# Kernel optimization log

Hardware: AMD Instinct MI355X
Metric: run time of the kernel (lower is better)

The kernel has to match this reference:

```python
import jax, jax.numpy as jnp
from jax import lax
import numpy as np

B, T, I, H, O = 128, 256, 256, 1024, 128


def _rnn_layer(x, W_ih, W_hh, b_ih, b_hh):
    # x: [B, T, D_in] -> hidden states [B, T, H]
    # precompute input projection for all timesteps (batched GEMM)
    xW = jnp.einsum('btd,hd->bth', x, W_ih) + b_ih + b_hh  # [B, T, H]

    def step(h, xw_t):
        h = jnp.tanh(xw_t + h @ W_hh.T)  # [B, H]
        return h, h

    h0 = jnp.zeros((x.shape[0], W_hh.shape[0]), x.dtype)
    _, hs = lax.scan(step, h0, jnp.swapaxes(xW, 0, 1))  # hs: [T, B, H]
    return jnp.swapaxes(hs, 0, 1)  # [B, T, H]


def setup_inputs() -> dict:
    key = jax.random.key(0)
    ks = jax.random.split(key, 11)
    s_ih0 = 1.0 / np.sqrt(H)
    inp = {
        'X': jax.random.normal(ks[0], (B, T, I), jnp.float32),
        'W_ih0': jax.random.uniform(ks[1], (H, I), jnp.float32, -s_ih0, s_ih0),
        'W_hh0': jax.random.uniform(ks[2], (H, H), jnp.float32, -s_ih0, s_ih0),
        'b_ih0': jax.random.uniform(ks[3], (H,), jnp.float32, -s_ih0, s_ih0),
        'b_hh0': jax.random.uniform(ks[4], (H,), jnp.float32, -s_ih0, s_ih0),
        'W_ih1': jax.random.uniform(ks[5], (H, H), jnp.float32, -s_ih0, s_ih0),
        'W_hh1': jax.random.uniform(ks[6], (H, H), jnp.float32, -s_ih0, s_ih0),
        'b_ih1': jax.random.uniform(ks[7], (H,), jnp.float32, -s_ih0, s_ih0),
        'b_hh1': jax.random.uniform(ks[8], (H,), jnp.float32, -s_ih0, s_ih0),
        'W_fc': jax.random.uniform(ks[9], (O, H), jnp.float32, -s_ih0, s_ih0),
        'b_fc': jax.random.uniform(ks[10], (O,), jnp.float32, -s_ih0, s_ih0),
    }
    return inp


def reference(X, W_ih0, W_hh0, b_ih0, b_hh0, W_ih1, W_hh1, b_ih1, b_hh1, W_fc, b_fc):
    h1 = _rnn_layer(X, W_ih0, W_hh0, b_ih0, b_hh0)   # layer 0: [B, T, H]
    h2 = _rnn_layer(h1, W_ih1, W_hh1, b_ih1, b_hh1)  # layer 1: [B, T, H]
    last = h2[:, -1, :]                               # [B, H]
    return last @ W_fc.T + b_fc                       # [B, O]
```

## Files before the change

kernel.cpp:

```cpp
#include <hip/hip_runtime.h>
#include <stdint.h>
#include <stddef.h>

#define B_ 128
#define T_ 256
#define I_ 256
#define H_ 1024
#define O_ 128

typedef __attribute__((ext_vector_type(8))) __bf16 bf16x8;
typedef __attribute__((ext_vector_type(4))) float f32x4;
typedef unsigned long long u64;
typedef unsigned int u32;



__global__ void split_kernel(const float* __restrict__ src, __bf16* __restrict__ hi,
                             __bf16* __restrict__ lo, int n) {
    int i = blockIdx.x * blockDim.x + threadIdx.x;
    int stride = gridDim.x * blockDim.x;
    for (; i < n; i += stride) {
        float v = src[i];
        __bf16 h = (__bf16)v;
        hi[i] = h;
        lo[i] = (__bf16)(v - (float)h);
    }
}

__global__ void pack_x(const float* __restrict__ X, u32* __restrict__ xp) {
    int i = blockIdx.x * 256 + threadIdx.x;
    int dw   = i & 3;
    int ln   = (i >> 2) & 15;
    int k8   = (i >> 6) & 31;
    int bt16 = (i >> 11) & 7;
    int t    = i >> 14;
    int k = k8 * 8 + dw * 2;
    int b = bt16 * 16 + ln;
    long xo = (long)b * T_ * I_ + (long)t * I_ + k;
    union { __bf16 b; unsigned short u; } h0, h1;
    h0.b = (__bf16)X[xo];
    h1.b = (__bf16)X[xo + 1];
    xp[(long)t * 16384 + bt16 * 2048 + k8 * 64 + ln * 4 + dw] =
        (u32)h0.u | ((u32)h1.u << 16);
}

__global__ void bias_sum_kernel(const float* __restrict__ a, const float* __restrict__ b,
                                float* __restrict__ o, int n) {
    int i = blockIdx.x * blockDim.x + threadIdx.x;
    if (i < n) o[i] = a[i] + b[i];
}

__global__ void transpose_fc(const float* __restrict__ w, float* __restrict__ wt) {
    int i = blockIdx.x * blockDim.x + threadIdx.x;
    if (i < O_ * H_) {
        int o = i / H_, k = i - o * H_;
        wt[k * O_ + o] = w[i];
    }
}


__device__ __forceinline__ bf16x8 load_frag_sc1(const u64* p) {
    union { u64 d[2]; bf16x8 v; } r;
    r.d[0] = __hip_atomic_load((u64*)p,     __ATOMIC_RELAXED, __HIP_MEMORY_SCOPE_AGENT);
    r.d[1] = __hip_atomic_load((u64*)p + 1, __ATOMIC_RELAXED, __HIP_MEMORY_SCOPE_AGENT);
    return r.v;
}

template <int CPW, int SEG0CH, bool X0>
__device__ __forceinline__ void step_full(
    const u32* __restrict__ xA0,
    const u64* __restrict__ hA0,
    const u64* __restrict__ Sp,
    const bf16x8 (&wh)[CPW][2], const bf16x8 (&wl)[CPW][2],
    const float* __restrict__ bs,
    u32* __restrict__ So, u32* __restrict__ Qo,
    int bt, int jt, int w, float* red)
{
    const int lane = threadIdx.x & 63;
    const int ln = lane & 15;
    const int q  = lane >> 4;

    f32x4 acc[2][2][2];
    #pragma unroll
    for (int s = 0; s < 2; ++s)
        #pragma unroll
        for (int n = 0; n < 2; ++n)
            #pragma unroll
            for (int r = 0; r < 2; ++r)
                acc[s][n][r] = (f32x4){0.f, 0.f, 0.f, 0.f};

    #pragma unroll
    for (int c = 0; c < CPW; ++c) {
        int gC = w * CPW + c;
        bf16x8 ah[2];
        if (gC < SEG0CH) {
            if (X0) {
                #pragma unroll
                for (int s = 0; s < 2; ++s) {
                    long off = (long)(bt * 2 + s) * (SEG0CH * 256)
                             + (gC * 4 + q) * 64 + ln * 4;
                    union { uint4 u; bf16x8 v; } r;
                    r.u = *(const uint4*)(xA0 + off);
                    ah[s] = r.v;
                }
            } else {
                #pragma unroll
                for (int s = 0; s < 2; ++s) {
                    long idx = (long)(bt * 2 + s) * (SEG0CH * 128)
                             + (gC * 4 + q) * 32 + ln * 2;
                    ah[s] = load_frag_sc1(hA0 + idx);
                }
            }
        } else {
            #pragma unroll
            for (int s = 0; s < 2; ++s) {
                long idx = (long)(bt * 2 + s) * 4096
                         + ((gC - SEG0CH) * 4 + q) * 32 + ln * 2;
                ah[s] = load_frag_sc1(Sp + idx);
            }
        }
        #pragma unroll
        for (int s = 0; s < 2; ++s)
            #pragma unroll
            for (int n = 0; n < 2; ++n) {
                acc[s][n][0] = __builtin_amdgcn_mfma_f32_16x16x32_bf16(ah[s], wh[c][n], acc[s][n][0], 0, 0, 0);
                acc[s][n][1] = __builtin_amdgcn_mfma_f32_16x16x32_bf16(ah[s], wl[c][n], acc[s][n][1], 0, 0, 0);
            }
    }

    {
        float* my = red + w * 1056;
        #pragma unroll
        for (int s = 0; s < 2; ++s)
            #pragma unroll
            for (int n = 0; n < 2; ++n) {
                f32x4 sum = acc[s][n][0] + acc[s][n][1];
                #pragma unroll
                for (int r = 0; r < 4; ++r)
                    my[(s * 16 + q * 4 + r) * 33 + n * 16 + ln] = sum[r];
            }
    }
    __syncthreads();

    {
        int tid = threadIdx.x;
        int row = tid & 31;
        int jp  = tid >> 5;
        int c0 = jp * 2;
        float v0 = 0.f, v1 = 0.f;
        #pragma unroll
        for (int w8 = 0; w8 < 8; ++w8) {
            v0 += red[w8 * 1056 + row * 33 + c0];
            v1 += red[w8 * 1056 + row * 33 + c0 + 1];
        }
        int j0 = jt * 32 + c0;
        float h0 = tanhf(v0 + bs[j0]);
        float h1v = tanhf(v1 + bs[j0 + 1]);
        union { __bf16 b; unsigned short u; } a0, a1;
        a0.b = (__bf16)h0;
        a1.b = (__bf16)h1v;
        u32 pk = (u32)a0.u | ((u32)a1.u << 16);
        int bgrp = bt * 2 + (row >> 4);
        long uidx = (long)bgrp * 8192 + (jt * 4 + (jp >> 2)) * 64
                  + (row & 15) * 4 + (jp & 3);
        __hip_atomic_store(&So[uidx], pk, __ATOMIC_RELAXED, __HIP_MEMORY_SCOPE_AGENT);
        if (Qo)
            __hip_atomic_store(&Qo[uidx], pk, __ATOMIC_RELAXED, __HIP_MEMORY_SCOPE_AGENT);
    }
}

__device__ __forceinline__ void cohort_barrier(unsigned* bar, int cohort, int grp,
                                               unsigned tgt, bool pub_prog) {
    asm volatile("s_waitcnt vmcnt(0)" ::: "memory");
    __syncthreads();
    if (threadIdx.x == 0) {
        unsigned* base = bar + cohort * 1024;
        unsigned old = __hip_atomic_fetch_add(&base[grp * 32], 1u, __ATOMIC_RELAXED,
                                              __HIP_MEMORY_SCOPE_AGENT);
        if ((old & 15u) == 15u) {
            unsigned so = __hip_atomic_fetch_add(&base[256], 1u, __ATOMIC_RELAXED,
                                                 __HIP_MEMORY_SCOPE_AGENT);
            if ((so & 7u) == 7u) {
                #pragma unroll
                for (int g = 0; g < 8; ++g)
                    __hip_atomic_store(&base[512 + g * 32], tgt, __ATOMIC_RELAXED,
                                       __HIP_MEMORY_SCOPE_AGENT);
                if (pub_prog) {
                    #pragma unroll
                    for (int g = 0; g < 8; ++g)
                        __hip_atomic_store(&bar[2048 + g * 32], tgt, __ATOMIC_RELAXED,
                                           __HIP_MEMORY_SCOPE_AGENT);
                }
            }
        }
        while (__hip_atomic_load(&base[512 + grp * 32], __ATOMIC_RELAXED,
                                 __HIP_MEMORY_SCOPE_AGENT) < tgt)
            __builtin_amdgcn_s_sleep(2);
    }
    __syncthreads();
    asm volatile("" ::: "memory");
}

struct PArgs {
    const u32* xp;
    const __bf16 *Wi0h, *Wi0l, *Wr0h, *Wr0l;
    const __bf16 *Wi1h, *Wi1l, *Wr1h, *Wr1l;
    const float *bs0, *bs1;
    u32 *h1;
    u32 *s0a, *s0b, *s1a, *s1b;
    unsigned* bar;
};

__global__ __launch_bounds__(512, 2) void persistent_rnn(PArgs a) {
    __shared__ float red[8 * 1056];
    const int w = threadIdx.x >> 6;
    const int lane = threadIdx.x & 63;
    const int ln = lane & 15;
    const int q  = lane >> 4;
    const int layer = blockIdx.x >> 7;
    const int r7 = blockIdx.x & 127;
    const int grp = r7 & 7;
    const int jt = r7 & 31;
    const int bt = r7 >> 5;

    if (layer == 0) {
        bf16x8 wh[5][2], wl[5][2];
        #pragma unroll
        for (int c = 0; c < 5; ++c) {
            int gC = w * 5 + c;
            #pragma unroll
            for (int n = 0; n < 2; ++n) {
                int jr = jt * 32 + n * 16 + ln;
                if (gC < 8) {
                    wh[c][n] = *(const bf16x8*)(a.Wi0h + (long)jr * 256 + gC * 32 + q * 8);
                    wl[c][n] = *(const bf16x8*)(a.Wi0l + (long)jr * 256 + gC * 32 + q * 8);
                } else {
                    wh[c][n] = *(const bf16x8*)(a.Wr0h + (long)jr * 1024 + (gC - 8) * 32 + q * 8);
                    wl[c][n] = *(const bf16x8*)(a.Wr0l + (long)jr * 1024 + (gC - 8) * 32 + q * 8);
                }
            }
        }
        for (int t = 0; t < T_; ++t) {
            const u32* sin = (t & 1) ? a.s0b : a.s0a;
            u32* sout      = (t & 1) ? a.s0a : a.s0b;
            step_full<5, 8, true>(a.xp + (long)t * 16384, (const u64*)nullptr,
                                  (const u64*)sin, wh, wl, a.bs0,
                                  sout, a.h1 + (long)t * 65536, bt, jt, w, red);
            cohort_barrier(a.bar, 0, grp, (unsigned)(t + 1), true);
        }
    } else {
        bf16x8 wh[8][2], wl[8][2];
        #pragma unroll
        for (int c = 0; c < 8; ++c) {
            int gC = w * 8 + c;
            #pragma unroll
            for (int n = 0; n < 2; ++n) {
                int jr = jt * 32 + n * 16 + ln;
                if (gC < 32) {
                    wh[c][n] = *(const bf16x8*)(a.Wi1h + (long)jr * 1024 + gC * 32 + q * 8);
                    wl[c][n] = *(const bf16x8*)(a.Wi1l + (long)jr * 1024 + gC * 32 + q * 8);
                } else {
                    wh[c][n] = *(const bf16x8*)(a.Wr1h + (long)jr * 1024 + (gC - 32) * 32 + q * 8);
                    wl[c][n] = *(const bf16x8*)(a.Wr1l + (long)jr * 1024 + (gC - 32) * 32 + q * 8);
                }
            }
        }
        for (int t1 = 0; t1 < T_; ++t1) {
            if (threadIdx.x == 0) {
                while (__hip_atomic_load(&a.bar[2048 + grp * 32], __ATOMIC_RELAXED,
                                         __HIP_MEMORY_SCOPE_AGENT) < (unsigned)(t1 + 1))
                    __builtin_amdgcn_s_sleep(2);
            }
            __syncthreads();
            const u32* sin = (t1 & 1) ? a.s1b : a.s1a;
            u32* sout      = (t1 & 1) ? a.s1a : a.s1b;
            step_full<8, 32, false>((const u32*)nullptr,
                                    (const u64*)(a.h1 + (long)t1 * 65536),
                                    (const u64*)sin, wh, wl, a.bs1,
                                    sout, (u32*)nullptr, bt, jt, w, red);
            cohort_barrier(a.bar, 1, grp, (unsigned)(t1 + 1), false);
        }
    }
}

__global__ __launch_bounds__(128) void fc_kernel(const u32* __restrict__ sp,
                                                 const float* __restrict__ wt,
                                                 const float* __restrict__ bfc,
                                                 float* __restrict__ out) {
    int b = blockIdx.x;
    int o = threadIdx.x;
    int bgrp = b >> 4, ln = b & 15;
    float acc = 0.f;
    #pragma unroll 4
    for (int kp = 0; kp < H_ / 2; ++kp) {
        u32 v = sp[(long)bgrp * 8192 + (kp >> 2) * 64 + ln * 4 + (kp & 3)];
        union { unsigned short u; __bf16 bf; } e0, e1;
        e0.u = (unsigned short)(v & 0xFFFF);
        e1.u = (unsigned short)(v >> 16);
        acc += (float)e0.bf * wt[(2 * kp) * O_ + o]
             + (float)e1.bf * wt[(2 * kp + 1) * O_ + o];
    }
    out[b * O_ + o] = acc + bfc[o];
}


extern "C" void kernel_launch(void* const* d_in, const int* in_sizes, int n_in,
                              void* d_out, int out_size, void* d_ws, size_t ws_size,
                              hipStream_t stream) {
    const float* X     = (const float*)d_in[0];
    const float* Wih0  = (const float*)d_in[1];
    const float* Whh0  = (const float*)d_in[2];
    const float* bih0  = (const float*)d_in[3];
    const float* bhh0  = (const float*)d_in[4];
    const float* Wih1  = (const float*)d_in[5];
    const float* Whh1  = (const float*)d_in[6];
    const float* bih1  = (const float*)d_in[7];
    const float* bhh1  = (const float*)d_in[8];
    const float* Wfc   = (const float*)d_in[9];
    const float* bfc   = (const float*)d_in[10];
    float* out = (float*)d_out;

    char* p = (char*)d_ws;
    auto alloc = [&](size_t bytes) -> void* {
        void* r = (void*)p;
        p += (bytes + 255) & ~(size_t)255;
        return r;
    };
    const size_t nW0 = (size_t)H_ * I_;
    const size_t nW  = (size_t)H_ * H_;
    u32* xp      = (u32*)alloc((size_t)T_ * 16384 * 4);
    __bf16* W0h  = (__bf16*)alloc(nW0 * 2);
    __bf16* W0l  = (__bf16*)alloc(nW0 * 2);
    __bf16* Wh0h = (__bf16*)alloc(nW * 2);
    __bf16* Wh0l = (__bf16*)alloc(nW * 2);
    __bf16* Wi1h = (__bf16*)alloc(nW * 2);
    __bf16* Wi1l = (__bf16*)alloc(nW * 2);
    __bf16* Wh1h = (__bf16*)alloc(nW * 2);
    __bf16* Wh1l = (__bf16*)alloc(nW * 2);
    u32* h1   = (u32*)alloc((size_t)T_ * 65536 * 4);
    u32* s0a  = (u32*)alloc(65536 * 4);
    u32* s0b  = (u32*)alloc(65536 * 4);
    u32* s1a  = (u32*)alloc(65536 * 4);
    u32* s1b  = (u32*)alloc(65536 * 4);
    float* wfct = (float*)alloc((size_t)H_ * O_ * 4);
    float* bs0  = (float*)alloc((size_t)H_ * 4);
    float* bs1  = (float*)alloc((size_t)H_ * 4);
    unsigned* bar = (unsigned*)alloc(16384);
    (void)ws_size; (void)n_in; (void)in_sizes; (void)out_size;

    pack_x<<<16384, 256, 0, stream>>>(X, xp);
    split_kernel<<<512, 256, 0, stream>>>(Wih0, W0h, W0l, (int)nW0);
    split_kernel<<<1024, 256, 0, stream>>>(Whh0, Wh0h, Wh0l, (int)nW);
    split_kernel<<<1024, 256, 0, stream>>>(Wih1, Wi1h, Wi1l, (int)nW);
    split_kernel<<<1024, 256, 0, stream>>>(Whh1, Wh1h, Wh1l, (int)nW);
    bias_sum_kernel<<<4, 256, 0, stream>>>(bih0, bhh0, bs0, H_);
    bias_sum_kernel<<<4, 256, 0, stream>>>(bih1, bhh1, bs1, H_);
    transpose_fc<<<(O_ * H_ + 255) / 256, 256, 0, stream>>>(Wfc, wfct);

    hipMemsetAsync(s0a, 0, 65536 * 4, stream);
    hipMemsetAsync(s1a, 0, 65536 * 4, stream);
    hipMemsetAsync(bar, 0, 16384, stream);

    PArgs args;
    args.xp = xp;
    args.Wi0h = W0h; args.Wi0l = W0l; args.Wr0h = Wh0h; args.Wr0l = Wh0l;
    args.Wi1h = Wi1h; args.Wi1l = Wi1l; args.Wr1h = Wh1h; args.Wr1l = Wh1l;
    args.bs0 = bs0; args.bs1 = bs1;
    args.h1 = h1;
    args.s0a = s0a; args.s0b = s0b; args.s1a = s1a; args.s1b = s1b;
    args.bar = bar;
    void* kp[] = { &args };
    hipLaunchCooperativeKernel((void*)persistent_rnn, dim3(256), dim3(512), kp, 0, stream);

    fc_kernel<<<B_, O_, 0, stream>>>(s1a, wfct, bfc, out);
}
```

Baseline: 2.257 ms.

## Replace cohort barriers with per-batch-tile dataflow counters and full-history state buffers

Each step used to end in a hierarchical cohort barrier across all 128 blocks of a layer. That is replaced by per-timestep completion counters scoped to each batch tile (32 producer blocks). Every wave spins only on the counter it needs before loading state, lazily, just ahead of the chunk that consumes it, so computation on x or prior chunks can overlap the wait. State buffers become one per timestep instead of ping-ponged, which removes the write-after-read hazard that the barrier guarded, at the cost of more workspace memory. Layer 1 now waits on layer 0's per-tile counter rather than a global progress flag.

```diff
diff --git a/kernel.cpp b/kernel.cpp
--- a/kernel.cpp
+++ b/kernel.cpp
@@ -58,6 +58,14 @@
     }
 }
 
+__global__ void seed_done(u32* d0, u32* d1) {
+    int bt = threadIdx.x;
+    if (bt < 4) {
+        d0[(bt * (T_ + 1)) * 32] = 32u;
+        d1[(bt * (T_ + 1)) * 32] = 32u;
+    }
+}
+
 
 __device__ __forceinline__ bf16x8 load_frag_sc1(const u64* p) {
     union { u64 d[2]; bf16x8 v; } r;
@@ -66,11 +74,18 @@
     return r.v;
 }
 
+__device__ __forceinline__ void spin_ge(const u32* c, u32 tgt) {
+    while (__hip_atomic_load((u32*)c, __ATOMIC_RELAXED, __HIP_MEMORY_SCOPE_AGENT) < tgt)
+        __builtin_amdgcn_s_sleep(2);
+    asm volatile("" ::: "memory");
+}
+
 template <int CPW, int SEG0CH, bool X0>
 __device__ __forceinline__ void step_full(
     const u32* __restrict__ xA0,
     const u64* __restrict__ hA0,
     const u64* __restrict__ Sp,
+    const u32* cntA, const u32* cntS,
     const bf16x8 (&wh)[CPW][2], const bf16x8 (&wl)[CPW][2],
     const float* __restrict__ bs,
     u32* __restrict__ So, u32* __restrict__ Qo,
@@ -89,6 +104,7 @@
             for (int r = 0; r < 2; ++r)
                 acc[s][n][r] = (f32x4){0.f, 0.f, 0.f, 0.f};
 
+    bool wA = false, wS = false;
     #pragma unroll
     for (int c = 0; c < CPW; ++c) {
         int gC = w * CPW + c;
@@ -104,6 +120,7 @@
                     ah[s] = r.v;
                 }
             } else {
+                if (!wA) { spin_ge(cntA, 32u); wA = true; }
                 #pragma unroll
                 for (int s = 0; s < 2; ++s) {
                     long idx = (long)(bt * 2 + s) * (SEG0CH * 128)
@@ -112,6 +129,7 @@
                 }
             }
         } else {
+            if (!wS) { spin_ge(cntS, 32u); wS = true; }
             #pragma unroll
             for (int s = 0; s < 2; ++s) {
                 long idx = (long)(bt * 2 + s) * 4096
@@ -169,36 +187,11 @@
     }
 }
 
-__device__ __forceinline__ void cohort_barrier(unsigned* bar, int cohort, int grp,
-                                               unsigned tgt, bool pub_prog) {
+__device__ __forceinline__ void signal_done(u32* cnt) {
     asm volatile("s_waitcnt vmcnt(0)" ::: "memory");
     __syncthreads();
-    if (threadIdx.x == 0) {
-        unsigned* base = bar + cohort * 1024;
-        unsigned old = __hip_atomic_fetch_add(&base[grp * 32], 1u, __ATOMIC_RELAXED,
-                                              __HIP_MEMORY_SCOPE_AGENT);
-        if ((old & 15u) == 15u) {
-            unsigned so = __hip_atomic_fetch_add(&base[256], 1u, __ATOMIC_RELAXED,
-                                                 __HIP_MEMORY_SCOPE_AGENT);
-            if ((so & 7u) == 7u) {
-                #pragma unroll
-                for (int g = 0; g < 8; ++g)
-                    __hip_atomic_store(&base[512 + g * 32], tgt, __ATOMIC_RELAXED,
-                                       __HIP_MEMORY_SCOPE_AGENT);
-                if (pub_prog) {
-                    #pragma unroll
-                    for (int g = 0; g < 8; ++g)
-                        __hip_atomic_store(&bar[2048 + g * 32], tgt, __ATOMIC_RELAXED,
-                                           __HIP_MEMORY_SCOPE_AGENT);
-                }
-            }
-        }
-        while (__hip_atomic_load(&base[512 + grp * 32], __ATOMIC_RELAXED,
-                                 __HIP_MEMORY_SCOPE_AGENT) < tgt)
-            __builtin_amdgcn_s_sleep(2);
-    }
-    __syncthreads();
-    asm volatile("" ::: "memory");
+    if (threadIdx.x == 0)
+        __hip_atomic_fetch_add(cnt, 1u, __ATOMIC_RELAXED, __HIP_MEMORY_SCOPE_AGENT);
 }
 
 struct PArgs {
@@ -207,8 +200,8 @@
     const __bf16 *Wi1h, *Wi1l, *Wr1h, *Wr1l;
     const float *bs0, *bs1;
     u32 *h1;
-    u32 *s0a, *s0b, *s1a, *s1b;
-    unsigned* bar;
+    u32 *s0, *s1;
+    u32 *done0, *done1;
 };
 
 __global__ __launch_bounds__(512, 2) void persistent_rnn(PArgs a) {
@@ -219,7 +212,6 @@
     const int q  = lane >> 4;
     const int layer = blockIdx.x >> 7;
     const int r7 = blockIdx.x & 127;
-    const int grp = r7 & 7;
     const int jt = r7 & 31;
     const int bt = r7 >> 5;
 
@@ -240,13 +232,15 @@
                 }
             }
         }
+        u32* myDone = a.done0 + (long)bt * (T_ + 1) * 32;
         for (int t = 0; t < T_; ++t) {
-            const u32* sin = (t & 1) ? a.s0b : a.s0a;
-            u32* sout      = (t & 1) ? a.s0a : a.s0b;
             step_full<5, 8, true>(a.xp + (long)t * 16384, (const u64*)nullptr,
-                                  (const u64*)sin, wh, wl, a.bs0,
-                                  sout, a.h1 + (long)t * 65536, bt, jt, w, red);
-            cohort_barrier(a.bar, 0, grp, (unsigned)(t + 1), true);
+                                  (const u64*)(a.s0 + (long)t * 65536),
+                                  (const u32*)nullptr, myDone + (long)t * 32,
+                                  wh, wl, a.bs0,
+                                  a.s0 + (long)(t + 1) * 65536,
+                                  a.h1 + (long)t * 65536, bt, jt, w, red);
+            signal_done(myDone + (long)(t + 1) * 32);
         }
     } else {
         bf16x8 wh[8][2], wl[8][2];
@@ -265,20 +259,18 @@
                 }
             }
         }
+        u32* prodDone = a.done0 + (long)bt * (T_ + 1) * 32;
+        u32* myDone   = a.done1 + (long)bt * (T_ + 1) * 32;
         for (int t1 = 0; t1 < T_; ++t1) {
-            if (threadIdx.x == 0) {
-                while (__hip_atomic_load(&a.bar[2048 + grp * 32], __ATOMIC_RELAXED,
-                                         __HIP_MEMORY_SCOPE_AGENT) < (unsigned)(t1 + 1))
-                    __builtin_amdgcn_s_sleep(2);
-            }
-            __syncthreads();
-            const u32* sin = (t1 & 1) ? a.s1b : a.s1a;
-            u32* sout      = (t1 & 1) ? a.s1a : a.s1b;
             step_full<8, 32, false>((const u32*)nullptr,
                                     (const u64*)(a.h1 + (long)t1 * 65536),
-                                    (const u64*)sin, wh, wl, a.bs1,
-                                    sout, (u32*)nullptr, bt, jt, w, red);
-            cohort_barrier(a.bar, 1, grp, (unsigned)(t1 + 1), false);
+                                    (const u64*)(a.s1 + (long)t1 * 65536),
+                                    prodDone + (long)(t1 + 1) * 32,
+                                    myDone + (long)t1 * 32,
+                                    wh, wl, a.bs1,
+                                    a.s1 + (long)(t1 + 1) * 65536,
+                                    (u32*)nullptr, bt, jt, w, red);
+            signal_done(myDone + (long)(t1 + 1) * 32);
         }
     }
 }
@@ -338,14 +330,13 @@
     __bf16* Wh1h = (__bf16*)alloc(nW * 2);
     __bf16* Wh1l = (__bf16*)alloc(nW * 2);
     u32* h1   = (u32*)alloc((size_t)T_ * 65536 * 4);
-    u32* s0a  = (u32*)alloc(65536 * 4);
-    u32* s0b  = (u32*)alloc(65536 * 4);
-    u32* s1a  = (u32*)alloc(65536 * 4);
-    u32* s1b  = (u32*)alloc(65536 * 4);
+    u32* s0   = (u32*)alloc((size_t)(T_ + 1) * 65536 * 4);
+    u32* s1   = (u32*)alloc((size_t)(T_ + 1) * 65536 * 4);
     float* wfct = (float*)alloc((size_t)H_ * O_ * 4);
     float* bs0  = (float*)alloc((size_t)H_ * 4);
     float* bs1  = (float*)alloc((size_t)H_ * 4);
-    unsigned* bar = (unsigned*)alloc(16384);
+    u32* done0 = (u32*)alloc((size_t)4 * (T_ + 1) * 32 * 4);
+    u32* done1 = (u32*)alloc((size_t)4 * (T_ + 1) * 32 * 4);
     (void)ws_size; (void)n_in; (void)in_sizes; (void)out_size;
 
     pack_x<<<16384, 256, 0, stream>>>(X, xp);
@@ -357,20 +348,21 @@
     bias_sum_kernel<<<4, 256, 0, stream>>>(bih1, bhh1, bs1, H_);
     transpose_fc<<<(O_ * H_ + 255) / 256, 256, 0, stream>>>(Wfc, wfct);
 
-    hipMemsetAsync(s0a, 0, 65536 * 4, stream);
-    hipMemsetAsync(s1a, 0, 65536 * 4, stream);
-    hipMemsetAsync(bar, 0, 16384, stream);
+    hipMemsetAsync(s0, 0, 65536 * 4, stream);
+    hipMemsetAsync(s1, 0, 65536 * 4, stream);
+    hipMemsetAsync(done0, 0, (size_t)4 * (T_ + 1) * 32 * 4, stream);
+    hipMemsetAsync(done1, 0, (size_t)4 * (T_ + 1) * 32 * 4, stream);
+    seed_done<<<1, 8, 0, stream>>>(done0, done1);
 
     PArgs args;
     args.xp = xp;
     args.Wi0h = W0h; args.Wi0l = W0l; args.Wr0h = Wh0h; args.Wr0l = Wh0l;
     args.Wi1h = Wi1h; args.Wi1l = Wi1l; args.Wr1h = Wh1h; args.Wr1l = Wh1l;
     args.bs0 = bs0; args.bs1 = bs1;
-    args.h1 = h1;
-    args.s0a = s0a; args.s0b = s0b; args.s1a = s1a; args.s1b = s1b;
-    args.bar = bar;
+    args.h1 = h1; args.s0 = s0; args.s1 = s1;
+    args.done0 = done0; args.done1 = done1;
     void* kp[] = { &args };
     hipLaunchCooperativeKernel((void*)persistent_rnn, dim3(256), dim3(512), kp, 0, stream);
 
-    fc_kernel<<<B_, O_, 0, stream>>>(s1a, wfct, bfc, out);
-}
+    fc_kernel<<<B_, O_, 0, stream>>>(s1 + (long)T_ * 65536, wfct, bfc, out);
+}
```

New measurement: 2.337 ms. +3.5%, slower.
